# Performance work log

Hardware: AMD Instinct MI355X
Metric: run time of the kernel (lower is better)

## Reference

```python
import jax, jax.numpy as jnp
import numpy as np

N_WIN = 7      # regions per side (BiFormer nchw BRA default)
TOPK = 4       # routed regions per query region
NH = 1         # num_heads (RefNet_encoder uses num_heads=1)
EPS = 1e-5


def _resize(x, hw):
    n, c = x.shape[:2]
    # torch F.interpolate(mode='bilinear', align_corners=False)
    return jax.image.resize(x, (n, c, hw[0], hw[1]), method='bilinear', antialias=False)


def _conv1x1(x, w, b):
    return jnp.einsum('nchw,oc->nohw', x, w) + b[None, :, None, None]


def _ln2d(x, g, b):
    # LayerNorm over channel dim of NCHW
    mu = jnp.mean(x, axis=1, keepdims=True)
    var = jnp.var(x, axis=1, keepdims=True)
    return (x - mu) * jax.lax.rsqrt(var + EPS) * g[None, :, None, None] + b[None, :, None, None]


def _to_regions(t, nh):
    # (N,C,H,W) -> (N, nh, R, rs, hd) with R = n_win^2 regions, rs tokens/region
    n, c, h, w = t.shape
    hd = c // nh
    rh, rw = h // N_WIN, w // N_WIN
    t = t.reshape(n, nh, hd, N_WIN, rh, N_WIN, rw)
    return t.transpose(0, 1, 3, 5, 4, 6, 2).reshape(n, nh, N_WIN * N_WIN, rh * rw, hd)


def _from_regions(t, h, w):
    n, nh, _, _, hd = t.shape
    rh, rw = h // N_WIN, w // N_WIN
    t = t.reshape(n, nh, N_WIN, N_WIN, rh, rw, hd)
    return t.transpose(0, 1, 6, 2, 4, 3, 5).reshape(n, nh * hd, h, w)


def _dwconv(x, w, b):
    # depthwise 5x5 LePE conv, padding=2
    y = jax.lax.conv_general_dilated(x, w, (1, 1), 'SAME',
        dimension_numbers=('NCHW', 'OIHW', 'NCHW'), feature_group_count=x.shape[1])
    return y + b[None, :, None, None]


def _bra(x, mask, qkv_w, qkv_b, lepe_w, lepe_b, proj_w, proj_b):
    n, c, h, w = x.shape
    hd = c // NH
    scale = hd ** -0.5
    rh, rw = h // N_WIN, w // N_WIN
    rs = rh * rw
    R = N_WIN * N_WIN
    q, k, v = jnp.split(_conv1x1(x, qkv_w, qkv_b), 3, axis=1)
    # region-to-region routing graph on detached q/k (avg-pooled regions)
    qd = jax.lax.stop_gradient(q).reshape(n, c, N_WIN, rh, N_WIN, rw).mean(axis=(3, 5)).reshape(n, c, R)
    kd = jax.lax.stop_gradient(k).reshape(n, c, N_WIN, rh, N_WIN, rw).mean(axis=(3, 5)).reshape(n, c, R)
    a_r = jnp.einsum('ncp,ncq->npq', qd, kd)             # (n, R, R)
    idx = jax.lax.top_k(a_r, TOPK)[1]                     # (n, R, TOPK)
    # token-to-token attention within routed regions
    qr = _to_regions(q, NH)                               # (n, nh, R, rs, hd)
    kr = _to_regions(k, NH)
    vr = _to_regions(v, NH)
    gidx = idx[:, None, :, :, None, None]                 # (n,1,Rq,topk,1,1)
    kg = jnp.take_along_axis(kr[:, :, None], gidx, axis=3).reshape(n, NH, R, TOPK * rs, hd)
    vg = jnp.take_along_axis(vr[:, :, None], gidx, axis=3).reshape(n, NH, R, TOPK * rs, hd)
    attn = jnp.einsum('nhrqd,nhrkd->nhrqk', qr * scale, kg)
    # glass-mask additive bias, partitioned + gathered exactly like the keys
    mr = _to_regions(mask, 1)[..., 0]                     # (n,1,R,rs)
    mg = jnp.take_along_axis(mr[:, :, None], idx[:, None, :, :, None], axis=3)
    attn = attn + mg.reshape(n, 1, R, 1, TOPK * rs)
    attn = jax.nn.softmax(attn, axis=-1)
    out = jnp.einsum('nhrqk,nhrkd->nhrqd', attn, vg)
    out = _from_regions(out, h, w) + _dwconv(v, lepe_w, lepe_b)
    return _conv1x1(out, proj_w, proj_b)


def _block(x, mask, i, ln1_g, ln1_b, ln2_g, ln2_b, qkv_w, qkv_b, lepe_w, lepe_b,
           proj_w, proj_b, fc1_w, fc1_b, fc2_w, fc2_b):
    x = x + _bra(_ln2d(x, ln1_g[i], ln1_b[i]), mask, qkv_w[i], qkv_b[i],
                 lepe_w[i], lepe_b[i], proj_w[i], proj_b[i])
    h = jax.nn.gelu(_conv1x1(_ln2d(x, ln2_g[i], ln2_b[i]), fc1_w[i], fc1_b[i]), approximate=False)
    return x + _conv1x1(h, fc2_w[i], fc2_b[i])


def reference(exemplar0, exemplar, input1, exemplar_pre, conv0_w, conv0_b,
              ln1_g, ln1_b, ln2_g, ln2_b, qkv_w, qkv_b, lepe_w, lepe_b,
              proj_w, proj_b, fc1_w, fc1_b, fc2_w, fc2_b):
    hw = exemplar.shape[2:]
    pre_s = _resize(exemplar_pre, hw)
    feats_s = _resize(exemplar0, hw)
    img_s = _resize(input1, hw)
    x = jnp.concatenate([feats_s, exemplar, img_s], axis=1)
    hx = jax.lax.conv_general_dilated(x, conv0_w, (1, 1), 'SAME',
        dimension_numbers=('NCHW', 'OIHW', 'NCHW')) + conv0_b[None, :, None, None]
    m = (jax.nn.sigmoid(pre_s) > 0.5).astype(x.dtype)
    attn_mask = jnp.where(m == 0, jnp.float32(-100.0), jnp.float32(0.0)).astype(x.dtype)
    for i in range(4):
        hx = _block(hx, attn_mask, i, ln1_g, ln1_b, ln2_g, ln2_b, qkv_w, qkv_b,
                    lepe_w, lepe_b, proj_w, proj_b, fc1_w, fc1_b, fc2_w, fc2_b)
    return hx


def setup_inputs() -> dict:
    key = jax.random.key(0)
    ks = jax.random.split(key, 12)
    B, C, H, W = 4, 64, 112, 112
    s = 0.05
    return {
        'exemplar0': jax.random.normal(ks[0], (B, C, 224, 224), jnp.float32),
        'exemplar': jax.random.normal(ks[1], (B, C, H, W), jnp.float32),
        'input1': jax.random.normal(ks[2], (B, 3, 224, 224), jnp.float32),
        'exemplar_pre': jax.random.normal(ks[3], (B, 1, 224, 224), jnp.float32),
        'conv0_w': jax.random.normal(ks[4], (C, 2 * C + 3, 3, 3), jnp.float32) * s,
        'conv0_b': jnp.zeros((C,), jnp.float32),
        'ln1_g': jnp.ones((4, C), jnp.float32),
        'ln1_b': jnp.zeros((4, C), jnp.float32),
        'ln2_g': jnp.ones((4, C), jnp.float32),
        'ln2_b': jnp.zeros((4, C), jnp.float32),
        'qkv_w': jax.random.normal(ks[5], (4, 3 * C, C), jnp.float32) * s,
        'qkv_b': jnp.zeros((4, 3 * C), jnp.float32),
        'lepe_w': jax.random.normal(ks[6], (4, C, 1, 5, 5), jnp.float32) * s,
        'lepe_b': jnp.zeros((4, C), jnp.float32),
        'proj_w': jax.random.normal(ks[7], (4, C, C), jnp.float32) * s,
        'proj_b': jnp.zeros((4, C), jnp.float32),
        'fc1_w': jax.random.normal(ks[8], (4, 4 * C, C), jnp.float32) * s,
        'fc1_b': jnp.zeros((4, 4 * C), jnp.float32),
        'fc2_w': jax.random.normal(ks[9], (4, C, 4 * C), jnp.float32) * s,
        'fc2_b': jnp.zeros((4, C), jnp.float32),
    }
```

## Files before the change

### kernel.cpp

```cpp
#include <hip/hip_runtime.h>

#define HW 112
#define PP 12544
#define BB 4
#define RR 49
#define RS 256
#define GW 114
#define GP (GW*GW)
#define CK 160

typedef __bf16 bf16;
typedef __bf16 bf16x8 __attribute__((ext_vector_type(8)));
typedef __bf16 bf16x4 __attribute__((ext_vector_type(4)));
typedef float f32x4 __attribute__((ext_vector_type(4)));

__device__ __forceinline__ int swzg(int row, int halfcol, int rowbytes) {
  int byte = halfcol * 2;
  return row * rowbytes + (byte & ~127) + ((((byte >> 4) ^ row) & 7) * 16) + (byte & 15);
}
__device__ __forceinline__ int swz128(int row, int halfcol) { return swzg(row, halfcol, 128); }

__device__ __forceinline__ float gelu_fast(float x) {
  float y = 0.7978845608f * (x + 0.044715f * x * x * x);
  float t = __expf(-2.f * fabsf(y));
  float th = (1.f - t) / (1.f + t);
  th = copysignf(th, y);
  return 0.5f * x * (1.f + th);
}

__device__ __forceinline__ void gl_lds16(const void* g, void* l) {
  __builtin_amdgcn_global_load_lds((const __attribute__((address_space(1))) unsigned int*)g,
                                   (__attribute__((address_space(3))) unsigned int*)l, 16, 0, 0);
}
__device__ __forceinline__ void gl_lds4(const void* g, void* l) {
  __builtin_amdgcn_global_load_lds((const __attribute__((address_space(1))) unsigned int*)g,
                                   (__attribute__((address_space(3))) unsigned int*)l, 4, 0, 0);
}

__global__ __launch_bounds__(256) void k_ring(bf16* __restrict__ xct) {
  int t = blockIdx.x * 256 + threadIdx.x;
  if (t >= BB * 452 * 20) return;
  int c4 = t % 20; int rem = t / 20; int ri = rem % 452; int n = rem / 452;
  int hh, ww;
  if (ri < 114)      { hh = 0;   ww = ri; }
  else if (ri < 228) { hh = 113; ww = ri - 114; }
  else if (ri < 340) { hh = 1 + (ri - 228); ww = 0; }
  else               { hh = 1 + (ri - 340); ww = 113; }
  uint4 zz = {0, 0, 0, 0};
  *(uint4*)(xct + ((size_t)n * GP + hh * GW + ww) * CK + c4 * 8) = zz;
}

__global__ __launch_bounds__(256) void k_prep2(const float* __restrict__ ex0, const float* __restrict__ ex,
    const float* __restrict__ img, const float* __restrict__ pre,
    bf16* __restrict__ xct, float* __restrict__ maskr) {
  __shared__ bf16 sT2[64 * 168];
  int n = blockIdx.y;
  int p0 = blockIdx.x * 64;
  int tid = threadIdx.x;
  uint4 zz = {0, 0, 0, 0};
  for (int i2 = tid; i2 < 1344; i2 += 256) ((uint4*)sT2)[i2] = zz;
  __syncthreads();
  int l = tid & 63, g = tid >> 6;
  int p = p0 + l;
  int h = p / HW, w = p % HW;
  for (int c = g; c < 131; c += 4) {
    float val;
    if (c < 64) {
      const float* s = ex0 + (((size_t)(n * 64 + c)) * 224 + 2 * h) * 224 + 2 * w;
      val = 0.5f * (0.5f * (s[0] + s[224]) + 0.5f * (s[1] + s[225]));
    } else if (c < 128) {
      val = ex[((size_t)(n * 64 + (c - 64))) * PP + p];
    } else {
      const float* s = img + (((size_t)(n * 3 + (c - 128))) * 224 + 2 * h) * 224 + 2 * w;
      val = 0.5f * (0.5f * (s[0] + s[224]) + 0.5f * (s[1] + s[225]));
    }
    sT2[l * 168 + c] = (bf16)val;
  }
  if (tid < 64) {
    const float* s = pre + ((size_t)n * 224 + 2 * h) * 224 + 2 * w;
    float v = 0.5f * (0.5f * (s[0] + s[224]) + 0.5f * (s[1] + s[225]));
    int r = (h >> 4) * 7 + (w >> 4); int sIdx = (h & 15) * 16 + (w & 15);
    maskr[(n * RR + r) * RS + sIdx] = (v > 0.0f) ? 0.0f : -100.0f;
  }
  __syncthreads();
  for (int i2 = tid; i2 < 1280; i2 += 256) {
    int row = i2 / 20, ch = i2 % 20;
    int pr = p0 + row;
    int hh = pr / HW, ww = pr % HW;
    uint4 d = *(const uint4*)(sT2 + row * 168 + ch * 8);
    *(uint4*)(xct + ((size_t)n * GP + (hh + 1) * GW + ww + 1) * CK + ch * 8) = d;
  }
}

__global__ __launch_bounds__(256) void k_wt2(const float* __restrict__ w, bf16* __restrict__ wTb) {
  int t = blockIdx.x * 256 + threadIdx.x;
  if (t >= 9 * 5 * 64 * 32) return;
  int cc = t & 31; int o = (t >> 5) & 63; int ks = (t >> 11) % 5; int k = t / 10240;
  int c = ks * 32 + cc;
  wTb[t] = (bf16)((c < 131) ? w[((size_t)(o * 131) + c) * 9 + k] : 0.f);
}

__global__ __launch_bounds__(256) void k_wcvt(const float* __restrict__ s0, bf16* __restrict__ d0, int n0,
    const float* __restrict__ s1, bf16* __restrict__ d1, int n1,
    const float* __restrict__ s2, bf16* __restrict__ d2, int n2,
    const float* __restrict__ s3, bf16* __restrict__ d3, int n3) {
  int t = blockIdx.x * 256 + threadIdx.x;
  if (t < n0) { d0[t] = (bf16)s0[t]; return; }
  t -= n0;
  if (t < n1) { d1[t] = (bf16)s1[t]; return; }
  t -= n1;
  if (t < n2) { d2[t] = (bf16)s2[t]; return; }
  t -= n2;
  if (t < n3) { d3[t] = (bf16)s3[t]; }
}

__global__ __launch_bounds__(256) void k_conv0m(const bf16* __restrict__ xct, const bf16* __restrict__ wTb,
    const float* __restrict__ bias, float* __restrict__ out_t) {
  __shared__ bf16 sA[128 * 32];
  __shared__ bf16 sB[64 * 32];
  int n = blockIdx.y;
  int p0 = blockIdx.x * 128;
  int tid = threadIdx.x, lane = tid & 63, wv = tid >> 6;
  int lo = lane & 15, hi = lane >> 4;
  size_t gofsA[2];
  #pragma unroll
  for (int it = 0; it < 2; it++) {
    int idx = tid + it * 256;
    int row = idx >> 2, ch = idx & 3;
    int p = p0 + row;
    int hh = p / HW, ww = p % HW;
    gofsA[it] = ((size_t)(hh + 1) * GW + ww + 1) * (CK * 2) + ch * 16;
  }
  const char* xbase = (const char*)(xct + (size_t)n * GP * CK);
  f32x4 acc[2][4];
  #pragma unroll
  for (int mi = 0; mi < 2; mi++)
    #pragma unroll
    for (int ni = 0; ni < 4; ni++) acc[mi][ni] = (f32x4){0.f, 0.f, 0.f, 0.f};
  for (int tap = 0; tap < 9; tap++) {
    long shift = (long)((tap / 3 - 1) * GW + (tap % 3 - 1)) * (CK * 2);
    for (int ks = 0; ks < 5; ks++) {
      uint4 a0 = *(const uint4*)(xbase + gofsA[0] + shift + ks * 64);
      uint4 a1 = *(const uint4*)(xbase + gofsA[1] + shift + ks * 64);
      uint4 b0 = *(const uint4*)((const char*)wTb + ((size_t)(tap * 5 + ks) * 2048 + tid * 8) * 2);
      __syncthreads();
      *(uint4*)((char*)sA + tid * 16) = a0;
      *(uint4*)((char*)sA + (tid + 256) * 16) = a1;
      *(uint4*)((char*)sB + tid * 16) = b0;
      __syncthreads();
      bf16x8 aF[2], bF[4];
      #pragma unroll
      for (int mi = 0; mi < 2; mi++)
        aF[mi] = *(const bf16x8*)((const char*)sA + (wv * 32 + mi * 16 + lo) * 64 + hi * 16);
      #pragma unroll
      for (int ni = 0; ni < 4; ni++)
        bF[ni] = *(const bf16x8*)((const char*)sB + (ni * 16 + lo) * 64 + hi * 16);
      #pragma unroll
      for (int mi = 0; mi < 2; mi++)
        #pragma unroll
        for (int ni = 0; ni < 4; ni++)
          acc[mi][ni] = __builtin_amdgcn_mfma_f32_16x16x32_bf16(aF[mi], bF[ni], acc[mi][ni], 0, 0, 0);
    }
  }
  #pragma unroll
  for (int ni = 0; ni < 4; ni++) {
    float bv = bias[ni * 16 + lo];
    #pragma unroll
    for (int mi = 0; mi < 2; mi++) {
      #pragma unroll
      for (int r2 = 0; r2 < 4; r2++) {
        int p = p0 + wv * 32 + mi * 16 + hi * 4 + r2;
        out_t[((size_t)n * PP + p) * 64 + ni * 16 + lo] = acc[mi][ni][r2] + bv;
      }
    }
  }
}

__global__ __launch_bounds__(512) void k_qkvr(const float* __restrict__ xin, const float* __restrict__ lng,
    const float* __restrict__ lnb, const bf16* __restrict__ wb, const float* __restrict__ bias,
    bf16* __restrict__ qRo, bf16* __restrict__ kRo, bf16* __restrict__ vto, bf16* __restrict__ vTo,
    float* __restrict__ qd, float* __restrict__ kd) {
  __shared__ __align__(16) char smem[45056];
  bf16* sA = (bf16*)smem;
  bf16* sB = (bf16*)(smem + 32768);
  float* rq = (float*)(smem + 40960);
  float* rk = (float*)(smem + 43008);
  bf16* sT = (bf16*)smem;
  int r = blockIdx.x, n = blockIdx.y;
  int nr = n * RR + r;
  int rh = (r / 7) * 16, rw = (r % 7) * 16;
  int tid = threadIdx.x, lane = tid & 63, wv = tid >> 6;
  int lo = lane & 15, hi = lane >> 4;
  {
    int row = tid >> 1, part = tid & 1;
    int y = row >> 4, x = row & 15;
    const float* xp = xin + ((size_t)n * PP + (rh + y) * HW + rw + x) * 64 + part * 32;
    float v[32]; float s = 0.f, sq = 0.f;
    #pragma unroll
    for (int i = 0; i < 8; i++) {
      float4 d = *(const float4*)&xp[i * 4];
      v[i*4]=d.x; v[i*4+1]=d.y; v[i*4+2]=d.z; v[i*4+3]=d.w;
      s += d.x+d.y+d.z+d.w;
      sq += d.x*d.x+d.y*d.y+d.z*d.z+d.w*d.w;
    }
    s += __shfl_xor(s, 1, 64); sq += __shfl_xor(sq, 1, 64);
    float mu = s * (1.f/64.f);
    float rstd = rsqrtf(fmaxf(sq * (1.f/64.f) - mu*mu, 0.f) + 1e-5f);
    #pragma unroll
    for (int j2 = 0; j2 < 4; j2++) {
      bf16x8 o8;
      #pragma unroll
      for (int e = 0; e < 8; e++) {
        int c = part*32 + j2*8 + e;
        o8[e] = (bf16)((v[j2*8+e] - mu) * rstd * lng[c] + lnb[c]);
      }
      *(bf16x8*)((char*)sA + swz128(row, part*32 + j2*8)) = o8;
    }
  }
  for (int ob = 0; ob < 3; ob++) {
    {
      int oo = tid >> 3, q8 = tid & 7;
      uint4 d = *(const uint4*)(wb + (size_t)(ob * 64 + oo) * 64 + q8 * 8);
      *(uint4*)((char*)sB + swz128(oo, q8 * 8)) = d;
    }
    __syncthreads();
    f32x4 acc[2][4];
    #pragma unroll
    for (int mi = 0; mi < 2; mi++)
      #pragma unroll
      for (int ni = 0; ni < 4; ni++) acc[mi][ni] = (f32x4){0.f, 0.f, 0.f, 0.f};
    #pragma unroll
    for (int kk = 0; kk < 2; kk++) {
      bf16x8 aF[2], bF[4];
      #pragma unroll
      for (int mi = 0; mi < 2; mi++)
        aF[mi] = *(const bf16x8*)((const char*)sA + swz128(wv * 32 + mi * 16 + lo, kk * 32 + hi * 8));
      #pragma unroll
      for (int ni = 0; ni < 4; ni++)
        bF[ni] = *(const bf16x8*)((const char*)sB + swz128(ni * 16 + lo, kk * 32 + hi * 8));
      #pragma unroll
      for (int mi = 0; mi < 2; mi++)
        #pragma unroll
        for (int ni = 0; ni < 4; ni++)
          acc[mi][ni] = __builtin_amdgcn_mfma_f32_16x16x32_bf16(aF[mi], bF[ni], acc[mi][ni], 0, 0, 0);
    }
    float bv[4];
    #pragma unroll
    for (int ni = 0; ni < 4; ni++) bv[ni] = bias[ob * 64 + ni * 16 + lo];
    if (ob == 0) {
      float part_[4] = {0.f, 0.f, 0.f, 0.f};
      #pragma unroll
      for (int ni = 0; ni < 4; ni++) {
        #pragma unroll
        for (int mi = 0; mi < 2; mi++) {
          #pragma unroll
          for (int r2 = 0; r2 < 4; r2++) {
            float rv = acc[mi][ni][r2] + bv[ni];
            int s = wv * 32 + mi * 16 + hi * 4 + r2;
            qRo[((size_t)nr * RS + s) * 64 + ni * 16 + lo] = (bf16)(rv * 0.125f);
            part_[ni] += rv;
          }
        }
        part_[ni] += __shfl_xor(part_[ni], 16, 64);
        part_[ni] += __shfl_xor(part_[ni], 32, 64);
        if (hi == 0) rq[wv * 64 + ni * 16 + lo] = part_[ni];
      }
      __syncthreads();
    } else if (ob == 1) {
      float part_[4] = {0.f, 0.f, 0.f, 0.f};
      #pragma unroll
      for (int ni = 0; ni < 4; ni++) {
        #pragma unroll
        for (int mi = 0; mi < 2; mi++) {
          #pragma unroll
          for (int r2 = 0; r2 < 4; r2++) {
            float rv = acc[mi][ni][r2] + bv[ni];
            int s = wv * 32 + mi * 16 + hi * 4 + r2;
            kRo[((size_t)nr * RS + s) * 64 + ni * 16 + lo] = (bf16)rv;
            part_[ni] += rv;
          }
        }
        part_[ni] += __shfl_xor(part_[ni], 16, 64);
        part_[ni] += __shfl_xor(part_[ni], 32, 64);
        if (hi == 0) rk[wv * 64 + ni * 16 + lo] = part_[ni];
      }
      __syncthreads();
    } else {
      __syncthreads();
      #pragma unroll
      for (int ni = 0; ni < 4; ni++) {
        int ch = ni * 16 + lo;
        #pragma unroll
        for (int mi = 0; mi < 2; mi++) {
          #pragma unroll
          for (int r2 = 0; r2 < 4; r2++) {
            float rv = acc[mi][ni][r2] + bv[ni];
            int s = wv * 32 + mi * 16 + hi * 4 + r2;
            bf16 b = (bf16)rv;
            vto[((size_t)n * PP + (rh + (s >> 4)) * HW + rw + (s & 15)) * 64 + ch] = b;
            sT[ch * 264 + s] = b;
          }
        }
      }
      __syncthreads();
      #pragma unroll
      for (int it = 0; it < 4; it++) {
        int idx = tid + it * 512;
        int row = idx >> 5, ch8 = idx & 31;
        uint4 d = *(const uint4*)(sT + row * 264 + ch8 * 8);
        *(uint4*)(vTo + ((size_t)nr * 64 + row) * 256 + ch8 * 8) = d;
      }
      if (tid < 64) {
        int c = tid;
        float aq = 0.f, ak = 0.f;
        #pragma unroll
        for (int w8 = 0; w8 < 8; w8++) { aq += rq[w8 * 64 + c]; ak += rk[w8 * 64 + c]; }
        qd[(n * 64 + c) * RR + r] = aq * (1.f / 256.f);
        kd[(n * 64 + c) * RR + r] = ak * (1.f / 256.f);
      }
    }
  }
}

__global__ __launch_bounds__(64) void k_topk(const float* __restrict__ qd, const float* __restrict__ kd,
    int* __restrict__ gidx) {
  int pq = blockIdx.x, n = blockIdx.y;
  int j = threadIdx.x;
  float a = -3e38f;
  if (j < RR) {
    a = 0.f;
    for (int c = 0; c < 64; c++)
      a += qd[(n * 64 + c) * RR + pq] * kd[(n * 64 + c) * RR + j];
  }
  for (int t = 0; t < 4; t++) {
    float bv = a; int bj = j;
    #pragma unroll
    for (int d = 32; d >= 1; d >>= 1) {
      float ov = __shfl_xor(bv, d, 64);
      int oj = __shfl_xor(bj, d, 64);
      if (ov > bv || (ov == bv && oj < bj)) { bv = ov; bj = oj; }
    }
    if (j == 0) gidx[(n * RR + pq) * 4 + t] = bj;
    if (j == bj) a = -3e38f;
  }
}

__global__ __launch_bounds__(512, 6) void k_attn(const bf16* __restrict__ qR, const bf16* __restrict__ kR,
    const bf16* __restrict__ vT, const float* __restrict__ maskr, const int* __restrict__ gidx,
    bf16* __restrict__ attnRb) {
  __shared__ bf16 sKd[2][64 * 64];
  __shared__ bf16 sVd[2][64 * 64];
  __shared__ bf16 sP[8][16 * 64];
  __shared__ float sMaskB[2][64];
  int bid = blockIdx.x;
  int newid = (bid & 7) * 49 + (bid >> 3);
  int n = newid / (RR * 2); int rem = newid % (RR * 2); int r = rem >> 1, qsp = rem & 1;
  int tid = threadIdx.x, lane = tid & 63, wv = tid >> 6;
  int lo = lane & 15, hi = lane >> 4;
  int m0 = qsp * 128 + wv * 16;
  const bf16* qbase = qR + ((size_t)(n * RR + r)) * RS * 64;
  bf16x8 qF[2];
  #pragma unroll
  for (int kk = 0; kk < 2; kk++)
    qF[kk] = *(const bf16x8*)(qbase + (m0 + lo) * 64 + kk * 32 + hi * 8);

  int gofsK, gofsV;
  {
    int rowT = wv * 8 + (lane >> 3);
    int c4 = ((lane & 7) ^ rowT) & 7;
    gofsK = rowT * 128 + c4 * 16;
    gofsV = rowT * 512 + c4 * 16;
  }

  const int* gptr = gidx + (n * RR + r) * 4;
  int j0g = gptr[0], j1g = gptr[1], j2g = gptr[2], j3g = gptr[3];

  f32x4 zero4 = {0.f, 0.f, 0.f, 0.f};
  f32x4 Oacc[4];
  #pragma unroll
  for (int di = 0; di < 4; di++) Oacc[di] = zero4;
  float mrun = -3e38f, lrun = 0.f;

  #define ISSUE_TILE(JREG, SUB, BUF) do {                                            \
    const char* kb_ = (const char*)(kR + ((size_t)(n * RR + (JREG))) * RS * 64) + (SUB) * 8192; \
    const char* vb_ = (const char*)(vT + ((size_t)(n * RR + (JREG))) * 64 * RS) + (SUB) * 128;  \
    gl_lds16(kb_ + gofsK, (char*)sKd + (BUF) * 8192 + wv * 1024);                    \
    gl_lds16(vb_ + gofsV, (char*)sVd + (BUF) * 8192 + wv * 1024);                    \
    if (wv == 0) gl_lds4(maskr + ((size_t)(n * RR + (JREG))) * RS + (SUB) * 64 + lane, (char*)sMaskB[(BUF)]); \
  } while (0)

  ISSUE_TILE(j0g, 0, 0);

  for (int ts = 0; ts < 16; ts++) {
    int cur = ts & 1;
    asm volatile("s_waitcnt lgkmcnt(0)" ::: "memory");
    __builtin_amdgcn_s_barrier();
    __builtin_amdgcn_sched_barrier(0);
    if (ts < 15) {
      int nts = ts + 1;
      int jn = (nts < 8) ? (nts < 4 ? j0g : j1g) : (nts < 12 ? j2g : j3g);
      int nsub = nts & 3;
      ISSUE_TILE(jn, nsub, cur ^ 1);
      if (wv == 0) { asm volatile("s_waitcnt vmcnt(3)" ::: "memory"); }
      else         { asm volatile("s_waitcnt vmcnt(2)" ::: "memory"); }
    } else {
      asm volatile("s_waitcnt vmcnt(0)" ::: "memory");
    }
    __builtin_amdgcn_s_barrier();
    __builtin_amdgcn_sched_barrier(0);
    const char* sK = (const char*)sKd + cur * 8192;
    const char* sV = (const char*)sVd + cur * 8192;
    f32x4 Sacc[4];
    #pragma unroll
    for (int ni = 0; ni < 4; ni++) Sacc[ni] = zero4;
    #pragma unroll
    for (int kk = 0; kk < 2; kk++) {
      #pragma unroll
      for (int ni = 0; ni < 4; ni++) {
        bf16x8 kF = *(const bf16x8*)(sK + swz128(ni * 16 + lo, kk * 32 + hi * 8));
        Sacc[ni] = __builtin_amdgcn_mfma_f32_16x16x32_bf16(kF, qF[kk], Sacc[ni], 0, 0, 0);
      }
    }
    const float* mB = sMaskB[cur];
    float ml = -3e38f;
    #pragma unroll
    for (int ni = 0; ni < 4; ni++) {
      #pragma unroll
      for (int jj = 0; jj < 4; jj++) {
        float sv = Sacc[ni][jj] + mB[ni * 16 + hi * 4 + jj];
        Sacc[ni][jj] = sv;
        ml = fmaxf(ml, sv);
      }
    }
    ml = fmaxf(ml, __shfl_xor(ml, 16, 64));
    ml = fmaxf(ml, __shfl_xor(ml, 32, 64));
    float nm = fmaxf(mrun, ml);
    float sc = __expf(mrun - nm);
    float rs = 0.f;
    bf16* sPw = sP[wv];
    #pragma unroll
    for (int ni = 0; ni < 4; ni++) {
      #pragma unroll
      for (int jj = 0; jj < 4; jj++) {
        float pv = __expf(Sacc[ni][jj] - nm);
        rs += pv;
        *(bf16*)((char*)sPw + swz128(lo, ni * 16 + hi * 4 + jj)) = (bf16)pv;
      }
    }
    rs += __shfl_xor(rs, 16, 64);
    rs += __shfl_xor(rs, 32, 64);
    mrun = nm; lrun = lrun * sc + rs;
    float scq[4];
    #pragma unroll
    for (int jj = 0; jj < 4; jj++) scq[jj] = __shfl(sc, hi * 4 + jj, 16);
    #pragma unroll
    for (int di = 0; di < 4; di++)
      #pragma unroll
      for (int jj = 0; jj < 4; jj++) Oacc[di][jj] *= scq[jj];
    #pragma unroll
    for (int kk = 0; kk < 2; kk++) {
      bf16x8 pF = *(const bf16x8*)((const char*)sPw + swz128(lo, kk * 32 + hi * 8));
      #pragma unroll
      for (int di = 0; di < 4; di++) {
        bf16x8 vF = *(const bf16x8*)(sV + swz128(di * 16 + lo, kk * 32 + hi * 8));
        Oacc[di] = __builtin_amdgcn_mfma_f32_16x16x32_bf16(pF, vF, Oacc[di], 0, 0, 0);
      }
    }
  }
  #undef ISSUE_TILE
  __syncthreads();
  float inv = 1.f / lrun;
  float invq[4];
  #pragma unroll
  for (int jj = 0; jj < 4; jj++) invq[jj] = __shfl(inv, hi * 4 + jj, 16);
  bf16* sOut = (bf16*)sKd;
  #pragma unroll
  for (int jj = 0; jj < 4; jj++) {
    int row = wv * 16 + hi * 4 + jj;
    #pragma unroll
    for (int di = 0; di < 4; di++)
      sOut[row * 64 + di * 16 + lo] = (bf16)(Oacc[di][jj] * invq[jj]);
  }
  __syncthreads();
  bf16* dst = attnRb + (((size_t)(n * RR + r)) * RS + qsp * 128) * 64;
  #pragma unroll
  for (int it = 0; it < 2; it++) {
    int idx = tid + it * 512;
    *(uint4*)(dst + idx * 8) = *(const uint4*)(sOut + idx * 8);
  }
}

__global__ __launch_bounds__(512) void k_lepe3(const bf16* __restrict__ v_t, const bf16* __restrict__ attnRb,
    const float* __restrict__ lw, const float* __restrict__ lb,
    const bf16* __restrict__ pwb, const float* __restrict__ pb, float* __restrict__ xo) {
  __shared__ __align__(16) char smem[64000];
  bf16* sH = (bf16*)smem;
  float* sW = (float*)(smem + 57600);
  bf16* zA = (bf16*)smem;
  bf16* sBp = (bf16*)(smem + 32768);
  int r = blockIdx.x, n = blockIdx.y;
  int rh = (r / 7) * 16, rw = (r % 7) * 16;
  int tid = threadIdx.x, lane = tid & 63, wv = tid >> 6;
  int lo = lane & 15, hi = lane >> 4;
  for (int i = tid; i < 1600; i += 512) { int c = i / 25, k = i % 25; sW[k * 64 + c] = lw[c * 25 + k]; }
  for (int g = tid; g < 3200; g += 512) {
    int pix = g >> 3, c4 = g & 7;
    int yy = pix / 20, xx = pix % 20;
    int hh = rh + yy - 2, ww = rw + xx - 2;
    uint4 d = {0, 0, 0, 0};
    if ((unsigned)hh < HW && (unsigned)ww < HW)
      d = *(const uint4*)(v_t + ((size_t)n * PP + hh * HW + ww) * 64 + c4 * 8);
    *(uint4*)((char*)sH + pix * 144 + c4 * 16) = d;
  }
  __syncthreads();
  int pixel = tid >> 1, part = tid & 1;
  int y = pixel >> 4, x = pixel & 15;
  float acc[32];
  const bf16* ar = attnRb + (((size_t)(n * RR + r)) * RS + pixel) * 64 + part * 32;
  #pragma unroll
  for (int c8 = 0; c8 < 4; c8++) {
    bf16x8 av = *(const bf16x8*)(ar + c8 * 8);
    #pragma unroll
    for (int j = 0; j < 8; j++) acc[c8 * 8 + j] = lb[part * 32 + c8 * 8 + j] + (float)av[j];
  }
  for (int t25 = 0; t25 < 25; t25++) {
    int dh = t25 / 5, dw = t25 % 5;
    int pix = (y + dh) * 20 + (x + dw);
    #pragma unroll
    for (int c8 = 0; c8 < 4; c8++) {
      bf16x8 hv = *(const bf16x8*)((const char*)sH + pix * 144 + (part * 4 + c8) * 16);
      #pragma unroll
      for (int j = 0; j < 8; j++) acc[c8 * 8 + j] += (float)hv[j] * sW[t25 * 64 + part * 32 + c8 * 8 + j];
    }
  }
  __syncthreads();
  #pragma unroll
  for (int i = 0; i < 4; i++) {
    bf16x8 o8;
    #pragma unroll
    for (int j = 0; j < 8; j++) o8[j] = (bf16)acc[i * 8 + j];
    *(bf16x8*)((char*)zA + swz128(pixel, part * 32 + i * 8)) = o8;
  }
  {
    int oo = tid >> 3, q8 = tid & 7;
    uint4 d = *(const uint4*)(pwb + (size_t)oo * 64 + q8 * 8);
    *(uint4*)((char*)sBp + swz128(oo, q8 * 8)) = d;
  }
  __syncthreads();
  f32x4 acc2[2][4];
  #pragma unroll
  for (int mi = 0; mi < 2; mi++)
    #pragma unroll
    for (int ni = 0; ni < 4; ni++) acc2[mi][ni] = (f32x4){0.f, 0.f, 0.f, 0.f};
  #pragma unroll
  for (int kk = 0; kk < 2; kk++) {
    bf16x8 aF[2], bF[4];
    #pragma unroll
    for (int mi = 0; mi < 2; mi++)
      aF[mi] = *(const bf16x8*)((const char*)zA + swz128(wv * 32 + mi * 16 + lo, kk * 32 + hi * 8));
    #pragma unroll
    for (int ni = 0; ni < 4; ni++)
      bF[ni] = *(const bf16x8*)((const char*)sBp + swz128(ni * 16 + lo, kk * 32 + hi * 8));
    #pragma unroll
    for (int mi = 0; mi < 2; mi++)
      #pragma unroll
      for (int ni = 0; ni < 4; ni++)
        acc2[mi][ni] = __builtin_amdgcn_mfma_f32_16x16x32_bf16(aF[mi], bF[ni], acc2[mi][ni], 0, 0, 0);
  }
  #pragma unroll
  for (int ni = 0; ni < 4; ni++) {
    float bv = pb[ni * 16 + lo];
    #pragma unroll
    for (int mi = 0; mi < 2; mi++) {
      #pragma unroll
      for (int r2 = 0; r2 < 4; r2++) {
        int s = wv * 32 + mi * 16 + hi * 4 + r2;
        int p = (rh + (s >> 4)) * HW + rw + (s & 15);
        xo[((size_t)n * PP + p) * 64 + ni * 16 + lo] += acc2[mi][ni][r2] + bv;
      }
    }
  }
}

__global__ __launch_bounds__(256) void k_mlp(const float* __restrict__ xin, const float* __restrict__ lng,
    const float* __restrict__ lnb, const bf16* __restrict__ w1b, const float* __restrict__ b1,
    const bf16* __restrict__ w2b, const float* __restrict__ b2, float* __restrict__ xo) {
  __shared__ bf16 sA[64 * 64];
  __shared__ bf16 sW[128 * 64];
  __shared__ bf16 sHh[64 * 128];
  int n = blockIdx.y;
  int p0 = blockIdx.x * 64;
  int tid = threadIdx.x, lane = tid & 63, wv = tid >> 6;
  int lo = lane & 15, hi = lane >> 4;
  {
    int row = tid >> 2, part = tid & 3;
    const float* xp = xin + ((size_t)n * PP + p0 + row) * 64 + part * 16;
    float v[16]; float s = 0.f, sq = 0.f;
    #pragma unroll
    for (int i = 0; i < 4; i++) {
      float4 d = *(const float4*)&xp[i * 4];
      v[i*4]=d.x; v[i*4+1]=d.y; v[i*4+2]=d.z; v[i*4+3]=d.w;
      s += d.x+d.y+d.z+d.w;
      sq += d.x*d.x+d.y*d.y+d.z*d.z+d.w*d.w;
    }
    s += __shfl_xor(s, 1, 64); sq += __shfl_xor(sq, 1, 64);
    s += __shfl_xor(s, 2, 64); sq += __shfl_xor(sq, 2, 64);
    float mu = s * (1.f/64.f);
    float rstd = rsqrtf(fmaxf(sq * (1.f/64.f) - mu*mu, 0.f) + 1e-5f);
    #pragma unroll
    for (int j2 = 0; j2 < 2; j2++) {
      bf16x8 o8;
      #pragma unroll
      for (int e = 0; e < 8; e++) {
        int c = part*16 + j2*8 + e;
        o8[e] = (bf16)((v[j2*8+e] - mu) * rstd * lng[c] + lnb[c]);
      }
      *(bf16x8*)((char*)sA + swz128(row, part*16 + j2*8)) = o8;
    }
  }
  f32x4 oacc[4];
  #pragma unroll
  for (int ni = 0; ni < 4; ni++) oacc[ni] = (f32x4){0.f, 0.f, 0.f, 0.f};
  for (int half = 0; half < 2; half++) {
    #pragma unroll
    for (int it = 0; it < 4; it++) {
      int idx = tid + it * 256;
      int oo = idx >> 3, q8 = idx & 7;
      uint4 d = *(const uint4*)(w1b + (size_t)(half * 128 + oo) * 64 + q8 * 8);
      *(uint4*)((char*)sW + swz128(oo, q8 * 8)) = d;
    }
    __syncthreads();
    f32x4 hacc[8];
    #pragma unroll
    for (int ni = 0; ni < 8; ni++) hacc[ni] = (f32x4){0.f, 0.f, 0.f, 0.f};
    #pragma unroll
    for (int kk = 0; kk < 2; kk++) {
      bf16x8 aF = *(const bf16x8*)((const char*)sA + swz128(wv * 16 + lo, kk * 32 + hi * 8));
      #pragma unroll
      for (int ni = 0; ni < 8; ni++) {
        bf16x8 bF = *(const bf16x8*)((const char*)sW + swz128(ni * 16 + lo, kk * 32 + hi * 8));
        hacc[ni] = __builtin_amdgcn_mfma_f32_16x16x32_bf16(aF, bF, hacc[ni], 0, 0, 0);
      }
    }
    #pragma unroll
    for (int ni = 0; ni < 8; ni++) {
      float bv = b1[half * 128 + ni * 16 + lo];
      #pragma unroll
      for (int r2 = 0; r2 < 4; r2++) {
        float hval = gelu_fast(hacc[ni][r2] + bv);
        *(bf16*)((char*)sHh + swzg(wv * 16 + hi * 4 + r2, ni * 16 + lo, 256)) = (bf16)hval;
      }
    }
    __syncthreads();
    #pragma unroll
    for (int it = 0; it < 4; it++) {
      int idx = tid + it * 256;
      int oo = idx >> 4, q8 = idx & 15;
      uint4 d = *(const uint4*)(w2b + (size_t)oo * 256 + half * 128 + q8 * 8);
      *(uint4*)((char*)sW + swzg(oo, q8 * 8, 256)) = d;
    }
    __syncthreads();
    #pragma unroll
    for (int kk = 0; kk < 4; kk++) {
      bf16x8 aH = *(const bf16x8*)((const char*)sHh + swzg(wv * 16 + lo, kk * 32 + hi * 8, 256));
      #pragma unroll
      for (int ni = 0; ni < 4; ni++) {
        bf16x8 bF = *(const bf16x8*)((const char*)sW + swzg(ni * 16 + lo, kk * 32 + hi * 8, 256));
        oacc[ni] = __builtin_amdgcn_mfma_f32_16x16x32_bf16(aH, bF, oacc[ni], 0, 0, 0);
      }
    }
    __syncthreads();
  }
  #pragma unroll
  for (int ni = 0; ni < 4; ni++) {
    float bv = b2[ni * 16 + lo];
    #pragma unroll
    for (int r2 = 0; r2 < 4; r2++) {
      int p = p0 + wv * 16 + hi * 4 + r2;
      xo[((size_t)n * PP + p) * 64 + ni * 16 + lo] += oacc[ni][r2] + bv;
    }
  }
}

__global__ __launch_bounds__(256) void k_untr(const float* __restrict__ x_t, float* __restrict__ out) {
  __shared__ float tile[64][68];
  int n = blockIdx.y; int p0 = blockIdx.x * 64;
  int tid = threadIdx.x;
  #pragma unroll
  for (int it = 0; it < 4; it++) {
    int g = tid + it * 256;
    int row = g >> 4, q = g & 15;
    float4 d = *(const float4*)&x_t[((size_t)n * PP + p0 + row) * 64 + q * 4];
    *(float4*)&tile[row][q * 4] = d;
  }
  __syncthreads();
  #pragma unroll
  for (int it = 0; it < 4; it++) {
    int g = tid + it * 256;
    int c = g >> 4, q = g & 15;
    float4 v;
    v.x = tile[q * 4 + 0][c]; v.y = tile[q * 4 + 1][c];
    v.z = tile[q * 4 + 2][c]; v.w = tile[q * 4 + 3][c];
    *(float4*)&out[((size_t)(n * 64 + c)) * PP + p0 + q * 4] = v;
  }
}

extern "C" void kernel_launch(void* const* d_in, const int* in_sizes, int n_in,
                              void* d_out, int out_size, void* d_ws, size_t ws_size,
                              hipStream_t stream) {
  const float* ex0 = (const float*)d_in[0];
  const float* ex  = (const float*)d_in[1];
  const float* img = (const float*)d_in[2];
  const float* pre = (const float*)d_in[3];
  const float* c0w = (const float*)d_in[4];
  const float* c0b = (const float*)d_in[5];
  const float* ln1g = (const float*)d_in[6];
  const float* ln1b = (const float*)d_in[7];
  const float* ln2g = (const float*)d_in[8];
  const float* ln2b = (const float*)d_in[9];
  const float* qkvw = (const float*)d_in[10];
  const float* qkvb = (const float*)d_in[11];
  const float* lw = (const float*)d_in[12];
  const float* lb = (const float*)d_in[13];
  const float* pw = (const float*)d_in[14];
  const float* pb = (const float*)d_in[15];
  const float* f1w = (const float*)d_in[16];
  const float* f1b = (const float*)d_in[17];
  const float* f2w = (const float*)d_in[18];
  const float* f2b = (const float*)d_in[19];

  float* W = (float*)d_ws;
  size_t o = 0;
  bf16* xct = (bf16*)(W + o);  o += (size_t)BB * GP * CK / 2;
  float* x_t  = W + o;         o += 3211264;
  bf16* attnRb = (bf16*)(W + o); o += 1605632;
  bf16* v_t  = (bf16*)(W + o); o += 1605632;
  bf16* qR   = (bf16*)(W + o); o += 1605632;
  bf16* kR   = (bf16*)(W + o); o += 1605632;
  bf16* vT   = (bf16*)(W + o); o += 1605632;
  float* qd = W + o;           o += 12544;
  float* kd = W + o;           o += 12544;
  float* maskr = W + o;        o += 50176;
  bf16* wTb = (bf16*)(W + o);  o += 46080;
  bf16* qkvwb = (bf16*)(W + o); o += 24576;
  bf16* pwb   = (bf16*)(W + o); o += 8192;
  bf16* f1wb  = (bf16*)(W + o); o += 32768;
  bf16* f2wb  = (bf16*)(W + o); o += 32768;
  int* gidx = (int*)(W + o);   o += 784;

  k_ring<<<dim3((BB * 452 * 20 + 255) / 256), dim3(256), 0, stream>>>(xct);
  k_prep2<<<dim3(196, BB), dim3(256), 0, stream>>>(ex0, ex, img, pre, xct, maskr);
  k_wt2<<<dim3(360), dim3(256), 0, stream>>>(c0w, wTb);
  k_wcvt<<<dim3((49152 + 16384 + 65536 + 65536 + 255) / 256), dim3(256), 0, stream>>>(
      qkvw, qkvwb, 49152, pw, pwb, 16384, f1w, f1wb, 65536, f2w, f2wb, 65536);
  k_conv0m<<<dim3(98, BB), dim3(256), 0, stream>>>(xct, wTb, c0b, x_t);
  for (int i = 0; i < 4; i++) {
    k_qkvr<<<dim3(RR, BB), dim3(512), 0, stream>>>(x_t, ln1g + i * 64, ln1b + i * 64,
        qkvwb + (size_t)i * 192 * 64, qkvb + i * 192, qR, kR, v_t, vT, qd, kd);
    k_topk<<<dim3(RR, BB), dim3(64), 0, stream>>>(qd, kd, gidx);
    k_attn<<<dim3(BB * RR * 2), dim3(512), 0, stream>>>(qR, kR, vT, maskr, gidx, attnRb);
    k_lepe3<<<dim3(RR, BB), dim3(512), 0, stream>>>(v_t, attnRb, lw + (size_t)i * 64 * 25, lb + i * 64,
        pwb + (size_t)i * 64 * 64, pb + i * 64, x_t);
    k_mlp<<<dim3(196, BB), dim3(256), 0, stream>>>(x_t, ln2g + i * 64, ln2b + i * 64,
        f1wb + (size_t)i * 256 * 64, f1b + i * 256, f2wb + (size_t)i * 64 * 256, f2b + i * 64, x_t);
  }
  k_untr<<<dim3(196, BB), dim3(256), 0, stream>>>(x_t, (float*)d_out);
}
```

Measured before the change: 474.0 us.

## Split routed-region attention over KV halves with a separate combine kernel

The attention kernel now splits each query block's four routed key regions into two halves, doubling the grid from 392 to 784 blocks. Each block writes unnormalized fp32 partial outputs plus running max and sum to workspace. A new k_comb kernel merges the two halves with log-sum-exp rescaling and writes the bf16 attention output. This targets low occupancy on a GPU with many compute units, at the cost of an extra kernel launch and fp32 round-trip traffic for the partials.

New measurement: 514.2 us. +8.5%, slower.

```diff
diff --git a/kernel.cpp b/kernel.cpp
--- a/kernel.cpp
+++ b/kernel.cpp
@@ -347,14 +347,17 @@
 
 __global__ __launch_bounds__(512, 6) void k_attn(const bf16* __restrict__ qR, const bf16* __restrict__ kR,
     const bf16* __restrict__ vT, const float* __restrict__ maskr, const int* __restrict__ gidx,
-    bf16* __restrict__ attnRb) {
-  __shared__ bf16 sKd[2][64 * 64];
-  __shared__ bf16 sVd[2][64 * 64];
-  __shared__ bf16 sP[8][16 * 64];
-  __shared__ float sMaskB[2][64];
+    float* __restrict__ part, float* __restrict__ ml) {
+  __shared__ __align__(16) char smem[49664];
+  bf16* sKd = (bf16*)smem;
+  bf16* sVd = (bf16*)(smem + 16384);
+  bf16* sP  = (bf16*)(smem + 32768);
+  float* sMaskB = (float*)(smem + 49152);
+  float* sOutF = (float*)smem;
   int bid = blockIdx.x;
-  int newid = (bid & 7) * 49 + (bid >> 3);
-  int n = newid / (RR * 2); int rem = newid % (RR * 2); int r = rem >> 1, qsp = rem & 1;
+  int newid = (bid & 7) * 98 + (bid >> 3);
+  int n = newid / (RR * 4); int rem = newid % (RR * 4);
+  int r = rem >> 2; int q2 = rem & 3; int qsp = q2 >> 1, half = q2 & 1;
   int tid = threadIdx.x, lane = tid & 63, wv = tid >> 6;
   int lo = lane & 15, hi = lane >> 4;
   int m0 = qsp * 128 + wv * 16;
@@ -372,8 +375,8 @@
     gofsV = rowT * 512 + c4 * 16;
   }
 
-  const int* gptr = gidx + (n * RR + r) * 4;
-  int j0g = gptr[0], j1g = gptr[1], j2g = gptr[2], j3g = gptr[3];
+  const int* gptr = gidx + (n * RR + r) * 4 + 2 * half;
+  int j0g = gptr[0], j1g = gptr[1];
 
   f32x4 zero4 = {0.f, 0.f, 0.f, 0.f};
   f32x4 Oacc[4];
@@ -386,19 +389,19 @@
     const char* vb_ = (const char*)(vT + ((size_t)(n * RR + (JREG))) * 64 * RS) + (SUB) * 128;  \
     gl_lds16(kb_ + gofsK, (char*)sKd + (BUF) * 8192 + wv * 1024);                    \
     gl_lds16(vb_ + gofsV, (char*)sVd + (BUF) * 8192 + wv * 1024);                    \
-    if (wv == 0) gl_lds4(maskr + ((size_t)(n * RR + (JREG))) * RS + (SUB) * 64 + lane, (char*)sMaskB[(BUF)]); \
+    if (wv == 0) gl_lds4(maskr + ((size_t)(n * RR + (JREG))) * RS + (SUB) * 64 + lane, (char*)(sMaskB + (BUF) * 64)); \
   } while (0)
 
   ISSUE_TILE(j0g, 0, 0);
 
-  for (int ts = 0; ts < 16; ts++) {
+  for (int ts = 0; ts < 8; ts++) {
     int cur = ts & 1;
     asm volatile("s_waitcnt lgkmcnt(0)" ::: "memory");
     __builtin_amdgcn_s_barrier();
     __builtin_amdgcn_sched_barrier(0);
-    if (ts < 15) {
+    if (ts < 7) {
       int nts = ts + 1;
-      int jn = (nts < 8) ? (nts < 4 ? j0g : j1g) : (nts < 12 ? j2g : j3g);
+      int jn = (nts < 4) ? j0g : j1g;
       int nsub = nts & 3;
       ISSUE_TILE(jn, nsub, cur ^ 1);
       if (wv == 0) { asm volatile("s_waitcnt vmcnt(3)" ::: "memory"); }
@@ -421,23 +424,23 @@
         Sacc[ni] = __builtin_amdgcn_mfma_f32_16x16x32_bf16(kF, qF[kk], Sacc[ni], 0, 0, 0);
       }
     }
-    const float* mB = sMaskB[cur];
-    float ml = -3e38f;
+    const float* mB = sMaskB + cur * 64;
+    float ml_ = -3e38f;
     #pragma unroll
     for (int ni = 0; ni < 4; ni++) {
       #pragma unroll
       for (int jj = 0; jj < 4; jj++) {
         float sv = Sacc[ni][jj] + mB[ni * 16 + hi * 4 + jj];
         Sacc[ni][jj] = sv;
-        ml = fmaxf(ml, sv);
-      }
-    }
-    ml = fmaxf(ml, __shfl_xor(ml, 16, 64));
-    ml = fmaxf(ml, __shfl_xor(ml, 32, 64));
-    float nm = fmaxf(mrun, ml);
+        ml_ = fmaxf(ml_, sv);
+      }
+    }
+    ml_ = fmaxf(ml_, __shfl_xor(ml_, 16, 64));
+    ml_ = fmaxf(ml_, __shfl_xor(ml_, 32, 64));
+    float nm = fmaxf(mrun, ml_);
     float sc = __expf(mrun - nm);
     float rs = 0.f;
-    bf16* sPw = sP[wv];
+    bf16* sPw = sP + wv * 1024;
     #pragma unroll
     for (int ni = 0; ni < 4; ni++) {
       #pragma unroll
@@ -468,25 +471,68 @@
     }
   }
   #undef ISSUE_TILE
+  int bpart = ((n * RR + r) * 2 + qsp) * 2 + half;
+  if (hi == 0) {
+    int q = wv * 16 + lo;
+    ml[(size_t)bpart * 256 + q] = mrun;
+    ml[(size_t)bpart * 256 + 128 + q] = lrun;
+  }
   __syncthreads();
-  float inv = 1.f / lrun;
-  float invq[4];
-  #pragma unroll
-  for (int jj = 0; jj < 4; jj++) invq[jj] = __shfl(inv, hi * 4 + jj, 16);
-  bf16* sOut = (bf16*)sKd;
   #pragma unroll
   for (int jj = 0; jj < 4; jj++) {
     int row = wv * 16 + hi * 4 + jj;
     #pragma unroll
     for (int di = 0; di < 4; di++)
-      sOut[row * 64 + di * 16 + lo] = (bf16)(Oacc[di][jj] * invq[jj]);
+      sOutF[row * 64 + di * 16 + lo] = Oacc[di][jj];
   }
   __syncthreads();
-  bf16* dst = attnRb + (((size_t)(n * RR + r)) * RS + qsp * 128) * 64;
-  #pragma unroll
-  for (int it = 0; it < 2; it++) {
+  float* dst = part + (size_t)bpart * 8192;
+  #pragma unroll
+  for (int it = 0; it < 4; it++) {
     int idx = tid + it * 512;
-    *(uint4*)(dst + idx * 8) = *(const uint4*)(sOut + idx * 8);
+    *(uint4*)(dst + idx * 4) = ((const uint4*)sOutF)[idx];
+  }
+}
+
+__global__ __launch_bounds__(256) void k_comb(const float* __restrict__ part, const float* __restrict__ ml,
+    bf16* __restrict__ attnRb) {
+  int idx2 = blockIdx.x, n = blockIdx.y;
+  int r = idx2 >> 1, qsp = idx2 & 1;
+  int tid = threadIdx.x;
+  int row = tid >> 1, ph = tid & 1;
+  int b0 = ((n * RR + r) * 2 + qsp) * 2;
+  float m0 = ml[(size_t)b0 * 256 + row];
+  float l0 = ml[(size_t)b0 * 256 + 128 + row];
+  float m1 = ml[(size_t)(b0 + 1) * 256 + row];
+  float l1 = ml[(size_t)(b0 + 1) * 256 + 128 + row];
+  float M = fmaxf(m0, m1);
+  float e0 = __expf(m0 - M), e1 = __expf(m1 - M);
+  float L = l0 * e0 + l1 * e1;
+  float f0 = e0 / L, f1 = e1 / L;
+  const float* O0 = part + (size_t)b0 * 8192 + row * 64 + ph * 32;
+  const float* O1 = part + (size_t)(b0 + 1) * 8192 + row * 64 + ph * 32;
+  bf16* dst = attnRb + (((size_t)(n * RR + r)) * RS + qsp * 128 + row) * 64 + ph * 32;
+  #pragma unroll
+  for (int i = 0; i < 4; i++) {
+    float4 a = *(const float4*)(O0 + i * 4 + (i >> 1) * 8);
+    (void)a;
+  }
+  #pragma unroll
+  for (int g = 0; g < 4; g++) {
+    float4 a0 = *(const float4*)(O0 + g * 8);
+    float4 a1 = *(const float4*)(O0 + g * 8 + 4);
+    float4 c0 = *(const float4*)(O1 + g * 8);
+    float4 c1 = *(const float4*)(O1 + g * 8 + 4);
+    bf16x8 o8;
+    o8[0] = (bf16)(a0.x * f0 + c0.x * f1);
+    o8[1] = (bf16)(a0.y * f0 + c0.y * f1);
+    o8[2] = (bf16)(a0.z * f0 + c0.z * f1);
+    o8[3] = (bf16)(a0.w * f0 + c0.w * f1);
+    o8[4] = (bf16)(a1.x * f0 + c1.x * f1);
+    o8[5] = (bf16)(a1.y * f0 + c1.y * f1);
+    o8[6] = (bf16)(a1.z * f0 + c1.z * f1);
+    o8[7] = (bf16)(a1.w * f0 + c1.w * f1);
+    *(bf16x8*)(dst + g * 8) = o8;
   }
 }
 
@@ -738,6 +784,8 @@
   bf16* qR   = (bf16*)(W + o); o += 1605632;
   bf16* kR   = (bf16*)(W + o); o += 1605632;
   bf16* vT   = (bf16*)(W + o); o += 1605632;
+  float* part = W + o;         o += (size_t)BB * RR * 4 * 8192;
+  float* ml   = W + o;         o += (size_t)BB * RR * 4 * 256;
   float* qd = W + o;           o += 12544;
   float* kd = W + o;           o += 12544;
   float* maskr = W + o;        o += 50176;
@@ -758,7 +806,8 @@
     k_qkvr<<<dim3(RR, BB), dim3(512), 0, stream>>>(x_t, ln1g + i * 64, ln1b + i * 64,
         qkvwb + (size_t)i * 192 * 64, qkvb + i * 192, qR, kR, v_t, vT, qd, kd);
     k_topk<<<dim3(RR, BB), dim3(64), 0, stream>>>(qd, kd, gidx);
-    k_attn<<<dim3(BB * RR * 2), dim3(512), 0, stream>>>(qR, kR, vT, maskr, gidx, attnRb);
+    k_attn<<<dim3(BB * RR * 4), dim3(512), 0, stream>>>(qR, kR, vT, maskr, gidx, part, ml);
+    k_comb<<<dim3(RR * 2, BB), dim3(256), 0, stream>>>(part, ml, attnRb);
     k_lepe3<<<dim3(RR, BB), dim3(512), 0, stream>>>(v_t, attnRb, lw + (size_t)i * 64 * 25, lb + i * 64,
         pwb + (size_t)i * 64 * 64, pb + i * 64, x_t);
     k_mlp<<<dim3(196, BB), dim3(256), 0, stream>>>(x_t, ln2g + i * 64, ln2b + i * 64,
```
